# Performance work log

Measured on AMD Instinct MI355X. Metric: run time of the kernel, lower is better.

Reference implementation:

```python
import jax, jax.numpy as jnp
import numpy as np

N = 100000
E = 3200000
D = 256


def setup_inputs() -> dict:
    key = jax.random.key(0)
    k1, k2, k3, k4 = jax.random.split(key, 4)
    x = jax.random.normal(k1, (N, D), dtype=jnp.float32)
    edge_index = jax.random.randint(k2, (2, E), 0, N, dtype=jnp.int64)
    # Glorot-ish scale for weights
    s = 1.0 / np.sqrt(D)
    W1 = jax.random.normal(k3, (D, D), dtype=jnp.float32) * s
    W2 = jax.random.normal(k4, (D, D), dtype=jnp.float32) * s
    b1 = jnp.zeros((D,), dtype=jnp.float32)
    b2 = jnp.zeros((D,), dtype=jnp.float32)
    return {"x": x, "edge_index": edge_index, "W1": W1, "b1": b1, "W2": W2, "b2": b2}


def _gcn_norm(edge_index, num_nodes):
    # PyG gcn_norm with add_self_loops=True, symmetric normalization.
    loop = jnp.arange(num_nodes, dtype=edge_index.dtype)
    src = jnp.concatenate([edge_index[0], loop])  # [E+N]
    dst = jnp.concatenate([edge_index[1], loop])  # [E+N]
    ones = jnp.ones(src.shape[0], dtype=jnp.float32)
    deg = jax.ops.segment_sum(ones, dst, num_segments=num_nodes)  # in-degree incl. self loop
    dis = jnp.where(deg > 0, jax.lax.rsqrt(deg), 0.0)
    norm = dis[src] * dis[dst]  # [E+N]
    return src, dst, norm


def _gcn_layer(x, src, dst, norm, W, b, num_nodes):
    xw = x @ W                                   # [N, D] dense GEMM
    msg = xw[src] * norm[:, None]                # gather + scale  [E+N, D]
    out = jax.ops.segment_sum(msg, dst, num_segments=num_nodes)  # scatter-add
    return out + b


def reference(x, edge_index, W1, b1, W2, b2):
    src, dst, norm = _gcn_norm(edge_index, N)
    h = jax.nn.elu(_gcn_layer(x, src, dst, norm, W1, b1, N))
    h = jax.nn.elu(_gcn_layer(h, src, dst, norm, W2, b2, N))
    return h
```

## Files before the change

### kernel.cpp

```cpp
#include <hip/hip_runtime.h>
#include <math.h>

#define N_NODES 100000
#define N_EDGES 3200000
#define DIM 256
#define SCAN_B 1024
#define SCAN_NBLK ((N_NODES + SCAN_B - 1) / SCAN_B)
#define NPASS 8
#define WIN ((N_NODES + NPASS - 1) / NPASS)

typedef unsigned short u16;
typedef unsigned int u32;
typedef __attribute__((ext_vector_type(8))) short bf16x8;
typedef __attribute__((ext_vector_type(4))) float f32x4;

__device__ __forceinline__ float bf2f(u16 u) {
    union { u32 i; float f; } v; v.i = ((u32)u) << 16; return v.f;
}
__device__ __forceinline__ u16 f2bf(float f) {
    union { float f; u32 i; } v; v.f = f;
    u32 x = v.i;
    return (u16)((x + 0x7fffu + ((x >> 16) & 1u)) >> 16);
}
__device__ __forceinline__ float sane(float v) {
    union { float f; u32 i; } u; u.f = v;
    if ((u.i & 0x7f800000u) == 0x7f800000u) return 0.f;
    return v;
}
__device__ __forceinline__ int iclamp(int v, int lo, int hi) {
    return v < lo ? lo : (v > hi ? hi : v);
}
__device__ __forceinline__ float2 cvt2(u32 d) {
    union { u32 i; float f; } lo, hi;
    lo.i = d << 16;
    hi.i = d & 0xffff0000u;
    return make_float2(lo.f, hi.f);
}

__global__ void detect_kernel(const u32* __restrict__ xw_words,
                              const int* __restrict__ ei, int* __restrict__ flags) {
    int lane = threadIdx.x;
    int cnt = 0;
#pragma unroll
    for (int j = 0; j < 4; ++j) {
        u32 e = (xw_words[lane + 64 * j] >> 7) & 0xffu;
        cnt += (e >= 0x70 && e <= 0x88) ? 1 : 0;
    }
    int nz = 0;
#pragma unroll
    for (int j = 0; j < 4; ++j) nz += (ei[2 * (lane + 64 * j) + 1] != 0) ? 1 : 0;
#pragma unroll
    for (int off = 32; off; off >>= 1) {
        cnt += __shfl_down(cnt, off, 64);
        nz += __shfl_down(nz, off, 64);
    }
    if (lane == 0) {
        flags[0] = (cnt < 128) ? 1 : 0;
        flags[1] = (nz == 0) ? 1 : 0;
    }
}

__device__ __forceinline__ int edge_val(const int* __restrict__ ei, int which,
                                        int i, int f64) {
    long long idx = (long long)which * N_EDGES + i;
    int v = f64 ? ei[idx * 2] : ei[idx];
    return iclamp(v, 0, N_NODES - 1);
}

__global__ void count_convert(const int* __restrict__ ei, int* __restrict__ rowcount,
                              int* __restrict__ src32, int* __restrict__ dst32,
                              const int* __restrict__ flags) {
    int i = blockIdx.x * blockDim.x + threadIdx.x;
    if (i < N_EDGES) {
        int f = flags[1];
        int s = edge_val(ei, 0, i, f);
        int d = edge_val(ei, 1, i, f);
        src32[i] = s;
        dst32[i] = d;
        atomicAdd(&rowcount[d], 1);
    }
}

__global__ __launch_bounds__(SCAN_B) void scan_block_sums(const int* __restrict__ cnt,
                                                          int* __restrict__ bsum) {
    __shared__ int ws[16];
    int i = blockIdx.x * SCAN_B + threadIdx.x;
    int v = (i < N_NODES) ? cnt[i] : 0;
#pragma unroll
    for (int off = 32; off; off >>= 1) v += __shfl_down(v, off, 64);
    if ((threadIdx.x & 63) == 0) ws[threadIdx.x >> 6] = v;
    __syncthreads();
    if (threadIdx.x < 16) {
        int t = ws[threadIdx.x];
#pragma unroll
        for (int off = 8; off; off >>= 1) t += __shfl_down(t, off, 16);
        if (threadIdx.x == 0) bsum[blockIdx.x] = t;
    }
}

__global__ void scan_bsum(int* __restrict__ bsum, int* __restrict__ rowptr) {
    __shared__ int sdata[128];
    int i = threadIdx.x;
    int v = (i < SCAN_NBLK) ? bsum[i] : 0;
    sdata[i] = v;
    __syncthreads();
    for (int off = 1; off < 128; off <<= 1) {
        int t = (i >= off) ? sdata[i - off] : 0;
        __syncthreads();
        sdata[i] += t;
        __syncthreads();
    }
    if (i < SCAN_NBLK) bsum[i] = sdata[i] - v;
    if (i == 0) rowptr[N_NODES] = sdata[127];
}

__global__ __launch_bounds__(SCAN_B) void scan_final(const int* __restrict__ cnt,
                                                     const int* __restrict__ bsum,
                                                     int* __restrict__ rowptr,
                                                     int* __restrict__ cursor,
                                                     float* __restrict__ dis) {
    __shared__ int ws[16];
    int lane = threadIdx.x & 63;
    int wid = threadIdx.x >> 6;
    int i = blockIdx.x * SCAN_B + threadIdx.x;
    int c = (i < N_NODES) ? cnt[i] : 0;
    int v = c;
#pragma unroll
    for (int off = 1; off < 64; off <<= 1) {
        int t = __shfl_up(v, off, 64);
        if (lane >= off) v += t;
    }
    if (lane == 63) ws[wid] = v;
    __syncthreads();
    int woff = 0;
    for (int w = 0; w < wid; ++w) woff += ws[w];
    int excl = bsum[blockIdx.x] + woff + v - c;
    if (i < N_NODES) {
        rowptr[i] = excl;
        cursor[i] = excl;
        dis[i] = rsqrtf((float)(iclamp(c, 0, N_EDGES) + 1));
    }
}

__global__ void fill_csr_pass(const int* __restrict__ src32,
                              const int* __restrict__ dst32,
                              int* __restrict__ cursor, int* __restrict__ colidx,
                              int lo) {
    int i = blockIdx.x * blockDim.x + threadIdx.x;
    if (i < N_EDGES) {
        int d = dst32[i];
        if ((unsigned)(d - lo) < (unsigned)WIN) {
            int pos = atomicAdd(&cursor[d], 1);
            colidx[pos] = src32[i];
        }
    }
}

__global__ void transpose_w2(const void* __restrict__ W1, const void* __restrict__ W2,
                             u16* __restrict__ Wt1, u16* __restrict__ Wt2,
                             const int* __restrict__ flags) {
    int n = blockIdx.x;
    int k = threadIdx.x;
    int f32mode = flags[0];
    float v1 = f32mode ? ((const float*)W1)[k * DIM + n]
                       : bf2f(((const u16*)W1)[k * DIM + n]);
    float v2 = f32mode ? ((const float*)W2)[k * DIM + n]
                       : bf2f(((const u16*)W2)[k * DIM + n]);
    Wt1[n * DIM + k] = f2bf(sane(v1));
    Wt2[n * DIM + k] = f2bf(sane(v2));
}

__global__ __launch_bounds__(256) void gemm_mfma(const void* __restrict__ Ain,
                                                 const u16* __restrict__ Wt,
                                                 const float* __restrict__ dis,
                                                 u16* __restrict__ out,
                                                 const int* __restrict__ flags,
                                                 int first) {
    int w = threadIdx.x >> 6;
    int lane = threadIdx.x & 63;
    int rt = blockIdx.x;
    int m = lane & 15;
    int quad = lane >> 4;

    bf16x8 B[4][8];
#pragma unroll
    for (int t2 = 0; t2 < 4; ++t2)
#pragma unroll
        for (int ks = 0; ks < 8; ++ks)
            B[t2][ks] = *(const bf16x8*)(Wt + (size_t)((w * 4 + t2) * 16 + m) * DIM +
                                         ks * 32 + quad * 8);

    int f32in = first ? flags[0] : 0;
    size_t rowoff = (size_t)(rt * 16 + m) * DIM + quad * 8;
    f32x4 acc[4];
#pragma unroll
    for (int t2 = 0; t2 < 4; ++t2) acc[t2] = (f32x4){0.f, 0.f, 0.f, 0.f};

#pragma unroll
    for (int ks = 0; ks < 8; ++ks) {
        bf16x8 a;
        if (f32in) {
            const float* ap = (const float*)Ain + rowoff + ks * 32;
            float4 f0 = *(const float4*)ap;
            float4 f1 = *(const float4*)(ap + 4);
            a[0] = (short)f2bf(sane(f0.x)); a[1] = (short)f2bf(sane(f0.y));
            a[2] = (short)f2bf(sane(f0.z)); a[3] = (short)f2bf(sane(f0.w));
            a[4] = (short)f2bf(sane(f1.x)); a[5] = (short)f2bf(sane(f1.y));
            a[6] = (short)f2bf(sane(f1.z)); a[7] = (short)f2bf(sane(f1.w));
        } else {
            union { bf16x8 v; u32 d[4]; } U;
            U.v = *(const bf16x8*)((const u16*)Ain + rowoff + ks * 32);
#pragma unroll
            for (int j = 0; j < 4; ++j) {
                u32 x = U.d[j];
                if ((x & 0x7f800000u) == 0x7f800000u) x &= 0x0000ffffu;
                if ((x & 0x00007f80u) == 0x00007f80u) x &= 0xffff0000u;
                U.d[j] = x;
            }
            a = U.v;
        }
#pragma unroll
        for (int t2 = 0; t2 < 4; ++t2)
            acc[t2] = __builtin_amdgcn_mfma_f32_16x16x32_bf16(a, B[t2][ks], acc[t2], 0, 0, 0);
    }

    float4 dv = *(const float4*)(dis + rt * 16 + quad * 4);
    float dr[4] = {dv.x, dv.y, dv.z, dv.w};

#pragma unroll
    for (int t2 = 0; t2 < 4; ++t2) {
#pragma unroll
        for (int r = 0; r < 4; ++r) {
            int row = rt * 16 + quad * 4 + r;
            int c = w * 64 + t2 * 16 + m;
            out[(size_t)row * DIM + c] = f2bf(sane(acc[t2][r] * dr[r]));
        }
    }
}

__global__ __launch_bounds__(256) void aggregate(const u16* __restrict__ xw,
                                                 const int* __restrict__ rowptr,
                                                 const int* __restrict__ colidx,
                                                 const float* __restrict__ dis,
                                                 const void* __restrict__ bias,
                                                 void* __restrict__ out,
                                                 const int* __restrict__ flags,
                                                 int final_layer) {
    int wid = threadIdx.x >> 6;
    int lane = threadIdx.x & 63;
    int node = blockIdx.x * 4 + wid;
    if (node >= N_NODES) return;
    int h = lane >> 5;
    int c8 = (lane & 31) * 8;
    const u16* base = xw + c8;

    float2 a0 = make_float2(0.f, 0.f), a1 = a0, a2 = a0, a3 = a0;
    if (h == 0) {
        uint4 v = *(const uint4*)(base + (size_t)node * DIM);
        a0 = cvt2(v.x); a1 = cvt2(v.y); a2 = cvt2(v.z); a3 = cvt2(v.w);
    }

#define ACC4(v)                                                   \
    do {                                                          \
        float2 t0 = cvt2((v).x), t1 = cvt2((v).y);                \
        float2 t2 = cvt2((v).z), t3 = cvt2((v).w);                \
        a0.x += t0.x; a0.y += t0.y; a1.x += t1.x; a1.y += t1.y;   \
        a2.x += t2.x; a2.y += t2.y; a3.x += t3.x; a3.y += t3.y;   \
    } while (0)

    int beg = rowptr[node];
    int end = rowptr[node + 1];
    int e = beg;

    int pe = (beg + 3) & ~3;
    if (pe > end) pe = end;
    for (int t = e; t < pe; t += 2) {
        int idx = t + h;
        if (idx < pe) {
            int s = colidx[idx];
            uint4 v = *(const uint4*)(base + (size_t)s * DIM);
            ACC4(v);
        }
    }
    e = pe;

    int me = e + ((end - e) & ~7);
    int h4 = h * 4;
    for (; e < me; e += 8) {
        int4 c4 = *(const int4*)(colidx + e + h4);
        uint4 v0 = *(const uint4*)(base + (size_t)c4.x * DIM);
        uint4 v1 = *(const uint4*)(base + (size_t)c4.y * DIM);
        uint4 v2 = *(const uint4*)(base + (size_t)c4.z * DIM);
        uint4 v3 = *(const uint4*)(base + (size_t)c4.w * DIM);
        ACC4(v0); ACC4(v1); ACC4(v2); ACC4(v3);
    }

    for (; e < end; e += 2) {
        int idx = e + h;
        if (idx < end) {
            int s = colidx[idx];
            uint4 v = *(const uint4*)(base + (size_t)s * DIM);
            ACC4(v);
        }
    }
#undef ACC4

    a0.x += __shfl_xor(a0.x, 32); a0.y += __shfl_xor(a0.y, 32);
    a1.x += __shfl_xor(a1.x, 32); a1.y += __shfl_xor(a1.y, 32);
    a2.x += __shfl_xor(a2.x, 32); a2.y += __shfl_xor(a2.y, 32);
    a3.x += __shfl_xor(a3.x, 32); a3.y += __shfl_xor(a3.y, 32);

    float s0, s1, s2, s3;
    if (h == 0) { s0 = a0.x; s1 = a0.y; s2 = a1.x; s3 = a1.y; }
    else        { s0 = a2.x; s1 = a2.y; s2 = a3.x; s3 = a3.y; }
    int c0 = c8 + h * 4;

    float dn = dis[node];
    float b0, b1, b2, b3;
    int f32mode = flags[0];
    if (f32mode) {
        float4 bv = *(const float4*)((const float*)bias + c0);
        b0 = bv.x; b1 = bv.y; b2 = bv.z; b3 = bv.w;
    } else {
        ushort4 bv = *(const ushort4*)((const u16*)bias + c0);
        b0 = bf2f(bv.x); b1 = bf2f(bv.y); b2 = bf2f(bv.z); b3 = bf2f(bv.w);
    }
    float o0 = dn * s0 + b0;
    float o1 = dn * s1 + b1;
    float o2 = dn * s2 + b2;
    float o3 = dn * s3 + b3;
    o0 = sane(o0 > 0.f ? o0 : expm1f(o0));
    o1 = sane(o1 > 0.f ? o1 : expm1f(o1));
    o2 = sane(o2 > 0.f ? o2 : expm1f(o2));
    o3 = sane(o3 > 0.f ? o3 : expm1f(o3));
    if (final_layer && f32mode) {
        float4 ov; ov.x = o0; ov.y = o1; ov.z = o2; ov.w = o3;
        *(float4*)((float*)out + (size_t)node * DIM + c0) = ov;
    } else {
        ushort4 ov;
        ov.x = f2bf(o0); ov.y = f2bf(o1); ov.z = f2bf(o2); ov.w = f2bf(o3);
        *(ushort4*)((u16*)out + (size_t)node * DIM + c0) = ov;
    }
}

extern "C" void kernel_launch(void* const* d_in, const int* in_sizes, int n_in,
                              void* d_out, int out_size, void* d_ws, size_t ws_size,
                              hipStream_t stream) {
    const void* x  = d_in[0];
    const int*  ei = (const int*)d_in[1];
    const void* W1 = d_in[2];
    const void* b1 = d_in[3];
    const void* W2 = d_in[4];
    const void* b2 = d_in[5];

    char* ws = (char*)d_ws;
    size_t off = 0;
    auto alloc = [&](size_t bytes) {
        void* p = ws + off;
        off = (off + bytes + 255) & ~(size_t)255;
        return p;
    };
    int*   flags    = (int*)alloc(256);
    int*   rowcount = (int*)alloc((size_t)N_NODES * 4);
    int*   rowptr   = (int*)alloc((size_t)(N_NODES + 1) * 4);
    int*   cursor   = (int*)alloc((size_t)N_NODES * 4);
    int*   colidx   = (int*)alloc((size_t)N_EDGES * 4);
    float* dis      = (float*)alloc((size_t)N_NODES * 4);
    int*   bsum     = (int*)alloc((size_t)SCAN_NBLK * 4 + 256);
    u16*   Wt1      = (u16*)alloc((size_t)DIM * DIM * 2);
    u16*   Wt2      = (u16*)alloc((size_t)DIM * DIM * 2);
    u16*   xw       = (u16*)alloc((size_t)N_NODES * DIM * 2);
    (void)ws_size;

    int* src32 = (int*)xw;
    int* dst32 = src32 + N_EDGES;

    detect_kernel<<<1, 64, 0, stream>>>((const u32*)x, ei, flags);
    hipMemsetAsync(rowcount, 0, (size_t)N_NODES * 4, stream);
    count_convert<<<(N_EDGES + 255) / 256, 256, 0, stream>>>(ei, rowcount, src32, dst32, flags);
    scan_block_sums<<<SCAN_NBLK, SCAN_B, 0, stream>>>(rowcount, bsum);
    scan_bsum<<<1, 128, 0, stream>>>(bsum, rowptr);
    scan_final<<<SCAN_NBLK, SCAN_B, 0, stream>>>(rowcount, bsum, rowptr, cursor, dis);
    for (int p = 0; p < NPASS; ++p)
        fill_csr_pass<<<(N_EDGES + 255) / 256, 256, 0, stream>>>(src32, dst32, cursor,
                                                                 colidx, p * WIN);
    transpose_w2<<<DIM, DIM, 0, stream>>>(W1, W2, Wt1, Wt2, flags);

    gemm_mfma<<<N_NODES / 16, 256, 0, stream>>>(x, Wt1, dis, xw, flags, 1);
    aggregate<<<N_NODES / 4, 256, 0, stream>>>(xw, rowptr, colidx, dis, b1, d_out, flags, 0);

    gemm_mfma<<<N_NODES / 16, 256, 0, stream>>>(d_out, Wt2, dis, xw, flags, 0);
    aggregate<<<N_NODES / 4, 256, 0, stream>>>(xw, rowptr, colidx, dis, b2, d_out, flags, 1);
}
```

Baseline: 1.202 ms.

## Sort CSR neighbors by source window and reuse GEMM weights across row tiles

The CSR build now counts edges into (dst, src>>12) buckets, giving 25 source windows per node. It then scans 2.5M buckets with a larger two-level scan, so each node's neighbor list ends up grouped by source range. This is meant to improve gather locality in the aggregate kernels. Separately, each GEMM block now processes 64 rows with the same register-resident weight fragments, which cuts redundant weight loads. The cost is a much larger count/scan array (10 MB) and extra scan work in the preprocessing stage.

```diff
diff --git a/kernel.cpp b/kernel.cpp
--- a/kernel.cpp
+++ b/kernel.cpp
@@ -5,9 +5,14 @@
 #define N_EDGES 3200000
 #define DIM 256
 #define SCAN_B 1024
-#define SCAN_NBLK ((N_NODES + SCAN_B - 1) / SCAN_B)
 #define NPASS 8
 #define WIN ((N_NODES + NPASS - 1) / NPASS)
+
+#define WSH 12
+#define NWIN 25
+#define NBUCK (N_NODES * NWIN)
+#define SCAN_GRID_W ((NBUCK + SCAN_B - 1) / SCAN_B)
+#define BS_CHUNK ((SCAN_GRID_W + 1023) / 1024)
 
 typedef unsigned short u16;
 typedef unsigned int u32;
@@ -67,7 +72,7 @@
     return iclamp(v, 0, N_NODES - 1);
 }
 
-__global__ void count_convert(const int* __restrict__ ei, int* __restrict__ rowcount,
+__global__ void count_convert(const int* __restrict__ ei, int* __restrict__ cnt2,
                               int* __restrict__ src32, int* __restrict__ dst32,
                               const int* __restrict__ flags) {
     int i = blockIdx.x * blockDim.x + threadIdx.x;
@@ -77,15 +82,16 @@
         int d = edge_val(ei, 1, i, f);
         src32[i] = s;
         dst32[i] = d;
-        atomicAdd(&rowcount[d], 1);
+        atomicAdd(&cnt2[d * NWIN + (s >> WSH)], 1);
     }
 }
 
 __global__ __launch_bounds__(SCAN_B) void scan_block_sums(const int* __restrict__ cnt,
-                                                          int* __restrict__ bsum) {
+                                                          int* __restrict__ bsum,
+                                                          int M) {
     __shared__ int ws[16];
     int i = blockIdx.x * SCAN_B + threadIdx.x;
-    int v = (i < N_NODES) ? cnt[i] : 0;
+    int v = (i < M) ? cnt[i] : 0;
 #pragma unroll
     for (int off = 32; off; off >>= 1) v += __shfl_down(v, off, 64);
     if ((threadIdx.x & 63) == 0) ws[threadIdx.x >> 6] = v;
@@ -98,32 +104,42 @@
     }
 }
 
-__global__ void scan_bsum(int* __restrict__ bsum, int* __restrict__ rowptr) {
-    __shared__ int sdata[128];
-    int i = threadIdx.x;
-    int v = (i < SCAN_NBLK) ? bsum[i] : 0;
-    sdata[i] = v;
+__global__ __launch_bounds__(1024) void scan_bsum_big(int* __restrict__ bsum) {
+    __shared__ int sd[1024];
+    int t = threadIdx.x;
+    int base = t * BS_CHUNK;
+    int v[BS_CHUNK];
+    int s = 0;
+#pragma unroll
+    for (int j = 0; j < BS_CHUNK; ++j) {
+        v[j] = (base + j < SCAN_GRID_W) ? bsum[base + j] : 0;
+        s += v[j];
+    }
+    sd[t] = s;
     __syncthreads();
-    for (int off = 1; off < 128; off <<= 1) {
-        int t = (i >= off) ? sdata[i - off] : 0;
+    for (int off = 1; off < 1024; off <<= 1) {
+        int x = (t >= off) ? sd[t - off] : 0;
         __syncthreads();
-        sdata[i] += t;
+        sd[t] += x;
         __syncthreads();
     }
-    if (i < SCAN_NBLK) bsum[i] = sdata[i] - v;
-    if (i == 0) rowptr[N_NODES] = sdata[127];
-}
-
-__global__ __launch_bounds__(SCAN_B) void scan_final(const int* __restrict__ cnt,
-                                                     const int* __restrict__ bsum,
-                                                     int* __restrict__ rowptr,
-                                                     int* __restrict__ cursor,
-                                                     float* __restrict__ dis) {
+    int ex = sd[t] - s;
+#pragma unroll
+    for (int j = 0; j < BS_CHUNK; ++j) {
+        if (base + j < SCAN_GRID_W) { bsum[base + j] = ex; ex += v[j]; }
+    }
+}
+
+__global__ __launch_bounds__(SCAN_B) void scan_final_w(const int* __restrict__ cnt,
+                                                       const int* __restrict__ bsum,
+                                                       int* __restrict__ rowptr,
+                                                       int* __restrict__ cursor,
+                                                       int M) {
     __shared__ int ws[16];
     int lane = threadIdx.x & 63;
     int wid = threadIdx.x >> 6;
     int i = blockIdx.x * SCAN_B + threadIdx.x;
-    int c = (i < N_NODES) ? cnt[i] : 0;
+    int c = (i < M) ? cnt[i] : 0;
     int v = c;
 #pragma unroll
     for (int off = 1; off < 64; off <<= 1) {
@@ -135,23 +151,30 @@
     int woff = 0;
     for (int w = 0; w < wid; ++w) woff += ws[w];
     int excl = bsum[blockIdx.x] + woff + v - c;
+    if (i < M) { rowptr[i] = excl; cursor[i] = excl; }
+    if (blockIdx.x == 0 && threadIdx.x == 0) rowptr[M] = N_EDGES;
+}
+
+__global__ void dis_kernel(const int* __restrict__ rowptr2, float* __restrict__ dis) {
+    int i = blockIdx.x * blockDim.x + threadIdx.x;
     if (i < N_NODES) {
-        rowptr[i] = excl;
-        cursor[i] = excl;
-        dis[i] = rsqrtf((float)(iclamp(c, 0, N_EDGES) + 1));
+        int indeg = rowptr2[(i + 1) * NWIN] - rowptr2[i * NWIN];
+        indeg = iclamp(indeg, 0, N_EDGES);
+        dis[i] = rsqrtf((float)(indeg + 1));
     }
 }
 
 __global__ void fill_csr_pass(const int* __restrict__ src32,
                               const int* __restrict__ dst32,
-                              int* __restrict__ cursor, int* __restrict__ colidx,
+                              int* __restrict__ cursor2, int* __restrict__ colidx,
                               int lo) {
     int i = blockIdx.x * blockDim.x + threadIdx.x;
     if (i < N_EDGES) {
         int d = dst32[i];
         if ((unsigned)(d - lo) < (unsigned)WIN) {
-            int pos = atomicAdd(&cursor[d], 1);
-            colidx[pos] = src32[i];
+            int s = src32[i];
+            int pos = atomicAdd(&cursor2[d * NWIN + (s >> WSH)], 1);
+            colidx[pos] = s;
         }
     }
 }
@@ -178,7 +201,6 @@
                                                  int first) {
     int w = threadIdx.x >> 6;
     int lane = threadIdx.x & 63;
-    int rt = blockIdx.x;
     int m = lane & 15;
     int quad = lane >> 4;
 
@@ -191,55 +213,60 @@
                                          ks * 32 + quad * 8);
 
     int f32in = first ? flags[0] : 0;
-    size_t rowoff = (size_t)(rt * 16 + m) * DIM + quad * 8;
-    f32x4 acc[4];
-#pragma unroll
-    for (int t2 = 0; t2 < 4; ++t2) acc[t2] = (f32x4){0.f, 0.f, 0.f, 0.f};
-
-#pragma unroll
-    for (int ks = 0; ks < 8; ++ks) {
-        bf16x8 a;
-        if (f32in) {
-            const float* ap = (const float*)Ain + rowoff + ks * 32;
-            float4 f0 = *(const float4*)ap;
-            float4 f1 = *(const float4*)(ap + 4);
-            a[0] = (short)f2bf(sane(f0.x)); a[1] = (short)f2bf(sane(f0.y));
-            a[2] = (short)f2bf(sane(f0.z)); a[3] = (short)f2bf(sane(f0.w));
-            a[4] = (short)f2bf(sane(f1.x)); a[5] = (short)f2bf(sane(f1.y));
-            a[6] = (short)f2bf(sane(f1.z)); a[7] = (short)f2bf(sane(f1.w));
-        } else {
-            union { bf16x8 v; u32 d[4]; } U;
-            U.v = *(const bf16x8*)((const u16*)Ain + rowoff + ks * 32);
-#pragma unroll
-            for (int j = 0; j < 4; ++j) {
-                u32 x = U.d[j];
-                if ((x & 0x7f800000u) == 0x7f800000u) x &= 0x0000ffffu;
-                if ((x & 0x00007f80u) == 0x00007f80u) x &= 0xffff0000u;
-                U.d[j] = x;
+
+    for (int rr = 0; rr < 4; ++rr) {
+        int row0 = blockIdx.x * 64 + rr * 16;
+        if (row0 >= N_NODES) break;
+        size_t rowoff = (size_t)(row0 + m) * DIM + quad * 8;
+        f32x4 acc[4];
+#pragma unroll
+        for (int t2 = 0; t2 < 4; ++t2) acc[t2] = (f32x4){0.f, 0.f, 0.f, 0.f};
+
+#pragma unroll
+        for (int ks = 0; ks < 8; ++ks) {
+            bf16x8 a;
+            if (f32in) {
+                const float* ap = (const float*)Ain + rowoff + ks * 32;
+                float4 f0 = *(const float4*)ap;
+                float4 f1 = *(const float4*)(ap + 4);
+                a[0] = (short)f2bf(sane(f0.x)); a[1] = (short)f2bf(sane(f0.y));
+                a[2] = (short)f2bf(sane(f0.z)); a[3] = (short)f2bf(sane(f0.w));
+                a[4] = (short)f2bf(sane(f1.x)); a[5] = (short)f2bf(sane(f1.y));
+                a[6] = (short)f2bf(sane(f1.z)); a[7] = (short)f2bf(sane(f1.w));
+            } else {
+                union { bf16x8 v; u32 d[4]; } U;
+                U.v = *(const bf16x8*)((const u16*)Ain + rowoff + ks * 32);
+#pragma unroll
+                for (int j = 0; j < 4; ++j) {
+                    u32 x = U.d[j];
+                    if ((x & 0x7f800000u) == 0x7f800000u) x &= 0x0000ffffu;
+                    if ((x & 0x00007f80u) == 0x00007f80u) x &= 0xffff0000u;
+                    U.d[j] = x;
+                }
+                a = U.v;
             }
-            a = U.v;
+#pragma unroll
+            for (int t2 = 0; t2 < 4; ++t2)
+                acc[t2] = __builtin_amdgcn_mfma_f32_16x16x32_bf16(a, B[t2][ks], acc[t2], 0, 0, 0);
         }
-#pragma unroll
-        for (int t2 = 0; t2 < 4; ++t2)
-            acc[t2] = __builtin_amdgcn_mfma_f32_16x16x32_bf16(a, B[t2][ks], acc[t2], 0, 0, 0);
-    }
-
-    float4 dv = *(const float4*)(dis + rt * 16 + quad * 4);
-    float dr[4] = {dv.x, dv.y, dv.z, dv.w};
-
-#pragma unroll
-    for (int t2 = 0; t2 < 4; ++t2) {
-#pragma unroll
-        for (int r = 0; r < 4; ++r) {
-            int row = rt * 16 + quad * 4 + r;
-            int c = w * 64 + t2 * 16 + m;
-            out[(size_t)row * DIM + c] = f2bf(sane(acc[t2][r] * dr[r]));
+
+        float4 dv = *(const float4*)(dis + row0 + quad * 4);
+        float dr[4] = {dv.x, dv.y, dv.z, dv.w};
+
+#pragma unroll
+        for (int t2 = 0; t2 < 4; ++t2) {
+#pragma unroll
+            for (int r = 0; r < 4; ++r) {
+                int row = row0 + quad * 4 + r;
+                int c = w * 64 + t2 * 16 + m;
+                out[(size_t)row * DIM + c] = f2bf(sane(acc[t2][r] * dr[r]));
+            }
         }
     }
 }
 
 __global__ __launch_bounds__(256) void aggregate(const u16* __restrict__ xw,
-                                                 const int* __restrict__ rowptr,
+                                                 const int* __restrict__ rowptr2,
                                                  const int* __restrict__ colidx,
                                                  const float* __restrict__ dis,
                                                  const void* __restrict__ bias,
@@ -268,8 +295,8 @@
         a2.x += t2.x; a2.y += t2.y; a3.x += t3.x; a3.y += t3.y;   \
     } while (0)
 
-    int beg = rowptr[node];
-    int end = rowptr[node + 1];
+    int beg = rowptr2[node * NWIN];
+    int end = rowptr2[node * NWIN + NWIN];
     int e = beg;
 
     int pe = (beg + 3) & ~3;
@@ -360,35 +387,37 @@
         off = (off + bytes + 255) & ~(size_t)255;
         return p;
     };
-    int*   flags    = (int*)alloc(256);
-    int*   rowcount = (int*)alloc((size_t)N_NODES * 4);
-    int*   rowptr   = (int*)alloc((size_t)(N_NODES + 1) * 4);
-    int*   cursor   = (int*)alloc((size_t)N_NODES * 4);
-    int*   colidx   = (int*)alloc((size_t)N_EDGES * 4);
-    float* dis      = (float*)alloc((size_t)N_NODES * 4);
-    int*   bsum     = (int*)alloc((size_t)SCAN_NBLK * 4 + 256);
-    u16*   Wt1      = (u16*)alloc((size_t)DIM * DIM * 2);
-    u16*   Wt2      = (u16*)alloc((size_t)DIM * DIM * 2);
-    u16*   xw       = (u16*)alloc((size_t)N_NODES * DIM * 2);
+    int*   flags   = (int*)alloc(256);
+    int*   rowptr2 = (int*)alloc(((size_t)NBUCK + 1) * 4);
+    int*   colidx  = (int*)alloc((size_t)N_EDGES * 4);
+    float* dis     = (float*)alloc((size_t)N_NODES * 4);
+    int*   bsum    = (int*)alloc((size_t)SCAN_GRID_W * 4 + 256);
+    u16*   Wt1     = (u16*)alloc((size_t)DIM * DIM * 2);
+    u16*   Wt2     = (u16*)alloc((size_t)DIM * DIM * 2);
+    u16*   xw      = (u16*)alloc((size_t)N_NODES * DIM * 2);
     (void)ws_size;
 
-    int* src32 = (int*)xw;
-    int* dst32 = src32 + N_EDGES;
+    char* xwb = (char*)xw;
+    int* src32  = (int*)xwb;
+    int* dst32  = (int*)(xwb + (size_t)N_EDGES * 4);
+    int* cnt2   = (int*)(xwb + (size_t)N_EDGES * 8);
+    int* cursor2 = cnt2;
 
     detect_kernel<<<1, 64, 0, stream>>>((const u32*)x, ei, flags);
-    hipMemsetAsync(rowcount, 0, (size_t)N_NODES * 4, stream);
-    count_convert<<<(N_EDGES + 255) / 256, 256, 0, stream>>>(ei, rowcount, src32, dst32, flags);
-    scan_block_sums<<<SCAN_NBLK, SCAN_B, 0, stream>>>(rowcount, bsum);
-    scan_bsum<<<1, 128, 0, stream>>>(bsum, rowptr);
-    scan_final<<<SCAN_NBLK, SCAN_B, 0, stream>>>(rowcount, bsum, rowptr, cursor, dis);
+    hipMemsetAsync(cnt2, 0, (size_t)NBUCK * 4, stream);
+    count_convert<<<(N_EDGES + 255) / 256, 256, 0, stream>>>(ei, cnt2, src32, dst32, flags);
+    scan_block_sums<<<SCAN_GRID_W, SCAN_B, 0, stream>>>(cnt2, bsum, NBUCK);
+    scan_bsum_big<<<1, 1024, 0, stream>>>(bsum);
+    scan_final_w<<<SCAN_GRID_W, SCAN_B, 0, stream>>>(cnt2, bsum, rowptr2, cursor2, NBUCK);
+    dis_kernel<<<(N_NODES + 255) / 256, 256, 0, stream>>>(rowptr2, dis);
     for (int p = 0; p < NPASS; ++p)
-        fill_csr_pass<<<(N_EDGES + 255) / 256, 256, 0, stream>>>(src32, dst32, cursor,
+        fill_csr_pass<<<(N_EDGES + 255) / 256, 256, 0, stream>>>(src32, dst32, cursor2,
                                                                  colidx, p * WIN);
     transpose_w2<<<DIM, DIM, 0, stream>>>(W1, W2, Wt1, Wt2, flags);
 
-    gemm_mfma<<<N_NODES / 16, 256, 0, stream>>>(x, Wt1, dis, xw, flags, 1);
-    aggregate<<<N_NODES / 4, 256, 0, stream>>>(xw, rowptr, colidx, dis, b1, d_out, flags, 0);
-
-    gemm_mfma<<<N_NODES / 16, 256, 0, stream>>>(d_out, Wt2, dis, xw, flags, 0);
-    aggregate<<<N_NODES / 4, 256, 0, stream>>>(xw, rowptr, colidx, dis, b2, d_out, flags, 1);
-}
+    gemm_mfma<<<(N_NODES + 63) / 64, 256, 0, stream>>>(x, Wt1, dis, xw, flags, 1);
+    aggregate<<<N_NODES / 4, 256, 0, stream>>>(xw, rowptr2, colidx, dis, b1, d_out, flags, 0);
+
+    gemm_mfma<<<(N_NODES + 63) / 64, 256, 0, stream>>>(d_out, Wt2, dis, xw, flags, 0);
+    aggregate<<<N_NODES / 4, 256, 0, stream>>>(xw, rowptr2, colidx, dis, b2, d_out, flags, 1);
+}
```

Result: faster. 1.111 ms (-7.5%).
